# Kernel optimization log

Hardware: AMD Instinct MI355X
Metric: run time of the kernel (lower is better)

Reference implementation:

```python
import jax, jax.numpy as jnp
import numpy as np

KS = 5
SIGMA = 2.0
N_BINS = 50
MOMENTUM = 0.9
HALF_KS = (KS - 1) // 2


def _gaussian_kernel_window(ks=KS, sigma=SIGMA):
    # Replicates scipy.ndimage.gaussian_filter1d(delta, sigma, mode='reflect'),
    # then renormalizes, exactly as FDS._get_kernel_window does.
    half = (ks - 1) // 2
    base = np.zeros(ks, np.float32)
    base[half] = 1.0
    r = int(4.0 * sigma + 0.5)  # scipy default truncate=4.0
    j = np.arange(-r, r + 1)
    w = np.exp(-0.5 * (j / sigma) ** 2)
    w = w / w.sum()
    idx = np.arange(-r, ks + r)
    for _ in range(8):  # repeated 'reflect' (edge-excluding-center style: d c b a | a b c d | d c b a)
        idx = np.where(idx < 0, -idx - 1, idx)
        idx = np.where(idx >= ks, 2 * ks - 1 - idx, idx)
    xp = base[idx]
    out = np.array([float(np.dot(w, xp[i:i + 2 * r + 1])) for i in range(ks)], np.float32)
    return out / out.sum()


def setup_inputs() -> dict:
    key = jax.random.key(0)
    k1, k2, k3, k4 = jax.random.split(key, 4)
    N, D = 262144, 512
    features = jax.random.normal(k1, (N, D), dtype=jnp.float32)
    labels = jax.random.randint(k2, (N,), 0, N_BINS, dtype=jnp.int64)
    running_mean = jax.random.normal(k3, (N_BINS, D), dtype=jnp.float32)
    running_var = jax.random.uniform(k4, (N_BINS, D), dtype=jnp.float32) + 0.5
    num_samples_tracked = jnp.zeros((N_BINS,), dtype=jnp.float32)
    kernel_window = jnp.asarray(_gaussian_kernel_window(), dtype=jnp.float32)
    return {
        "features": features,
        "labels": labels,
        "running_mean": running_mean,
        "running_var": running_var,
        "num_samples_tracked": num_samples_tracked,
        "kernel_window": kernel_window,
    }


def _smooth(x, kernel_window):
    # reflect-pad (torch 'reflect': excludes edge) along bin axis, then cross-correlate (F.conv1d)
    top = x[HALF_KS:0:-1]              # [half_ks, D]
    bot = x[-2:-2 - HALF_KS:-1]        # [half_ks, D]
    xp = jnp.concatenate([top, x, bot], axis=0)  # [B + 2*half_ks, D]
    B = x.shape[0]
    windows = jnp.stack([xp[i:i + B] for i in range(KS)], axis=0)  # [ks, B, D]
    return jnp.einsum("k,kbd->bd", kernel_window, windows)


def reference(features, labels, running_mean, running_var, num_samples_tracked, kernel_window):
    # --- segmented per-bin mean/var (single pass, replaces the Python loop over labels) ---
    N = features.shape[0]
    labels = labels.astype(jnp.int32)
    counts = jax.ops.segment_sum(jnp.ones((N,), features.dtype), labels, num_segments=N_BINS)  # [B]
    sums = jax.ops.segment_sum(features, labels, num_segments=N_BINS)                          # [B, D]
    sumsq = jax.ops.segment_sum(features * features, labels, num_segments=N_BINS)              # [B, D]
    safe_n = jnp.maximum(counts, 1.0)
    mean = sums / safe_n[:, None]
    # unbiased var for n>1; biased (=0) for n==1, matching torch.var unbiased toggle
    var = (sumsq - safe_n[:, None] * mean * mean) / jnp.maximum(counts - 1.0, 1.0)[:, None]

    present = (counts > 0)[:, None]
    f = MOMENTUM
    new_mean = jnp.where(present, (1.0 - f) * mean + f * running_mean, running_mean)
    new_var = jnp.where(present, (1.0 - f) * var + f * running_var, running_var)
    new_num = num_samples_tracked + counts

    # --- update_smoothed_stats: conv1d smoothing over the bin axis ---
    smoothed_mean = _smooth(new_mean, kernel_window)
    smoothed_var = _smooth(new_var, kernel_window)
    return new_mean, new_var, new_num, smoothed_mean, smoothed_var
```

## Files before the change

kernel.cpp:

```cpp
#include <hip/hip_runtime.h>

#define NB 50
#define DD 512
#define KSZ 5
#define SORT_ROWS 4096
#define EPT 16
#define RPW 512
#define COLG 8
#define UNR 8

__global__ __launch_bounds__(256) void fds_sort(
    const int* __restrict__ labels,
    int*       __restrict__ packed,
    float*     __restrict__ g_cnt)
{
    __shared__ int s_hist[NB];
    __shared__ int s_cur[NB];
    const int tid  = threadIdx.x;
    const int base = blockIdx.x * SORT_ROWS;

    if (tid < NB) s_hist[tid] = 0;
    __syncthreads();

    int lab[EPT];
#pragma unroll
    for (int j = 0; j < EPT; ++j) {
        lab[j] = labels[base + j * 256 + tid];
        __hip_atomic_fetch_add(&s_hist[lab[j]], 1,
                               __ATOMIC_RELAXED, __HIP_MEMORY_SCOPE_WORKGROUP);
    }
    __syncthreads();

    if (tid == 0) {
        int run = 0;
        for (int b = 0; b < NB; ++b) { s_cur[b] = run; run += s_hist[b]; }
    }
    __syncthreads();

    if (tid < NB)
        __hip_atomic_fetch_add(&g_cnt[tid], (float)s_hist[tid],
                               __ATOMIC_RELAXED, __HIP_MEMORY_SCOPE_AGENT);

#pragma unroll
    for (int j = 0; j < EPT; ++j) {
        const int l   = lab[j];
        const int pos = __hip_atomic_fetch_add(&s_cur[l], 1,
                              __ATOMIC_RELAXED, __HIP_MEMORY_SCOPE_WORKGROUP);
        const int row = base + j * 256 + tid;
        packed[base + pos] = (row << 6) | l;
    }
}

__global__ __launch_bounds__(256) void fds_reduce(
    const float* __restrict__ features,
    const int*   __restrict__ packed,
    float* __restrict__ g_sum,
    float* __restrict__ g_sq)
{
    const int tid  = threadIdx.x;
    const int wave = tid >> 6;
    const int lane = tid & 63;
    const int gw   = blockIdx.x * 4 + wave;
    const int cg     = gw & (COLG - 1);
    const int rchunk = gw >> 3;
    const int col = cg * 64 + lane;
    const int r0  = rchunk * RPW;

    float sum = 0.f, sq = 0.f;
    int cur = packed[r0] & 63;

    int pk[UNR];
#pragma unroll
    for (int j = 0; j < UNR; ++j) pk[j] = packed[r0 + j];

    for (int it = 0; it < RPW; it += UNR) {
        float v[UNR];
#pragma unroll
        for (int j = 0; j < UNR; ++j)
            v[j] = features[(size_t)(pk[j] >> 6) * DD + col];

        int pk2[UNR];
        const int nb = (it + UNR < RPW) ? (r0 + it + UNR) : r0;
#pragma unroll
        for (int j = 0; j < UNR; ++j) pk2[j] = packed[nb + j];

#pragma unroll
        for (int j = 0; j < UNR; ++j) {
            const int l = pk[j] & 63;
            if (l != cur) {
                __hip_atomic_fetch_add(&g_sum[cur * DD + col], sum,
                                       __ATOMIC_RELAXED, __HIP_MEMORY_SCOPE_AGENT);
                __hip_atomic_fetch_add(&g_sq [cur * DD + col], sq,
                                       __ATOMIC_RELAXED, __HIP_MEMORY_SCOPE_AGENT);
                sum = 0.f; sq = 0.f; cur = l;
            }
            sum += v[j];
            sq = fmaf(v[j], v[j], sq);
        }
#pragma unroll
        for (int j = 0; j < UNR; ++j) pk[j] = pk2[j];
    }
    __hip_atomic_fetch_add(&g_sum[cur * DD + col], sum,
                           __ATOMIC_RELAXED, __HIP_MEMORY_SCOPE_AGENT);
    __hip_atomic_fetch_add(&g_sq [cur * DD + col], sq,
                           __ATOMIC_RELAXED, __HIP_MEMORY_SCOPE_AGENT);
}

__global__ __launch_bounds__(256) void fds_finalize(
    const float* __restrict__ g_sum, const float* __restrict__ g_sq,
    const float* __restrict__ g_cnt,
    const float* __restrict__ running_mean, const float* __restrict__ running_var,
    const float* __restrict__ num_tracked, const float* __restrict__ kwin,
    float* __restrict__ out)
{
    __shared__ float s_cnt[NB];
    __shared__ float s_w[KSZ];
    const int tid = threadIdx.x;
    if (tid < NB)  s_cnt[tid] = g_cnt[tid];
    if (tid < KSZ) s_w[tid]   = kwin[tid];
    __syncthreads();

    const int idx = blockIdx.x * 256 + tid;
    const int b = idx / DD;
    const int d = idx - b * DD;

    float sm = 0.f, sv = 0.f, my_nm = 0.f, my_nv = 0.f;
#pragma unroll
    for (int k = 0; k < KSZ; ++k) {
        const int i = b + k;
        const int bb = (i < 2) ? (2 - i) : ((i >= NB + 2) ? (2 * NB - i) : (i - 2));
        const float cnt    = s_cnt[bb];
        const float safe_n = fmaxf(cnt, 1.f);
        const float s   = g_sum[bb * DD + d];
        const float sqv = g_sq [bb * DD + d];
        const float mean = s / safe_n;
        const float var  = (sqv - safe_n * mean * mean) / fmaxf(cnt - 1.f, 1.f);
        const float rm = running_mean[bb * DD + d];
        const float rv = running_var [bb * DD + d];
        float nm, nv;
        if (cnt > 0.f) {
            nm = 0.1f * mean + 0.9f * rm;
            nv = 0.1f * var  + 0.9f * rv;
        } else {
            nm = rm; nv = rv;
        }
        sm += s_w[k] * nm;
        sv += s_w[k] * nv;
        if (k == 2) { my_nm = nm; my_nv = nv; }
    }
    out[idx]                    = my_nm;
    out[NB * DD + idx]          = my_nv;
    out[2 * NB * DD + NB + idx] = sm;
    out[3 * NB * DD + NB + idx] = sv;
    if (idx < NB)
        out[2 * NB * DD + idx] = num_tracked[idx] + s_cnt[idx];
}

extern "C" void kernel_launch(void* const* d_in, const int* in_sizes, int n_in,
                              void* d_out, int out_size, void* d_ws, size_t ws_size,
                              hipStream_t stream)
{
    const float* features     = (const float*)d_in[0];
    const int*   labels       = (const int*)  d_in[1];
    const float* running_mean = (const float*)d_in[2];
    const float* running_var  = (const float*)d_in[3];
    const float* num_tracked  = (const float*)d_in[4];
    const float* kwin         = (const float*)d_in[5];
    float* out = (float*)d_out;

    const int N = in_sizes[1];

    float* g_sum  = (float*)d_ws;
    float* g_sq   = g_sum + NB * DD;
    float* g_cnt  = g_sq  + NB * DD;
    int*   packed = (int*)(g_cnt + NB);

    hipMemsetAsync(d_ws, 0, (size_t)(2 * NB * DD + NB) * sizeof(float), stream);

    fds_sort<<<N / SORT_ROWS, 256, 0, stream>>>(labels, packed, g_cnt);

    fds_reduce<<<(N / RPW) * COLG / 4, 256, 0, stream>>>(features, packed, g_sum, g_sq);

    fds_finalize<<<NB * DD / 256, 256, 0, stream>>>(
        g_sum, g_sq, g_cnt, running_mean, running_var, num_tracked, kwin, out);
}
```

Baseline: 710.2 us.

## Vectorize reduce to float4 loads with nontemporal hints and shorter row chunks

Reworks the segmented reduction so each lane loads four contiguous columns as a float4, and one wave covers half a row (256 columns) instead of 64. Feature loads are marked nontemporal because the feature stream is read once. The rows per wave drop from 512 to 64 and the grid is resized to match. The aim is fewer, wider memory transactions and more parallelism for the 512 MB feature stream. In exchange, the shorter chunks produce more bin boundaries and so more global atomic flushes, four scalar atomics per accumulator each time.

New measurement: 709.4 us. Within noise of the previous version (-0.1%).

```diff
diff --git a/kernel.cpp b/kernel.cpp
--- a/kernel.cpp
+++ b/kernel.cpp
@@ -5,9 +5,10 @@
 #define KSZ 5
 #define SORT_ROWS 4096
 #define EPT 16
-#define RPW 512
-#define COLG 8
+#define RPW 64
 #define UNR 8
+
+typedef float f4 __attribute__((ext_vector_type(4)));
 
 __global__ __launch_bounds__(256) void fds_sort(
     const int* __restrict__ labels,
@@ -51,6 +52,21 @@
     }
 }
 
+__device__ __forceinline__ void flush4(
+    float* __restrict__ g_sum, float* __restrict__ g_sq,
+    int cur, int c0, f4 sum, f4 sq)
+{
+    float* ps = &g_sum[cur * DD + c0];
+    float* pq = &g_sq [cur * DD + c0];
+#pragma unroll
+    for (int c = 0; c < 4; ++c) {
+        __hip_atomic_fetch_add(ps + c, sum[c],
+                               __ATOMIC_RELAXED, __HIP_MEMORY_SCOPE_AGENT);
+        __hip_atomic_fetch_add(pq + c, sq[c],
+                               __ATOMIC_RELAXED, __HIP_MEMORY_SCOPE_AGENT);
+    }
+}
+
 __global__ __launch_bounds__(256) void fds_reduce(
     const float* __restrict__ features,
     const int*   __restrict__ packed,
@@ -61,12 +77,13 @@
     const int wave = tid >> 6;
     const int lane = tid & 63;
     const int gw   = blockIdx.x * 4 + wave;
-    const int cg     = gw & (COLG - 1);
-    const int rchunk = gw >> 3;
-    const int col = cg * 64 + lane;
+    const int cg2    = gw & 1;
+    const int rchunk = gw >> 1;
     const int r0  = rchunk * RPW;
+    const int c0  = cg2 * 256 + lane * 4;
+    const f4* __restrict__ f4p = (const f4*)features;
 
-    float sum = 0.f, sq = 0.f;
+    f4 sum = (f4)0.f, sq = (f4)0.f;
     int cur = packed[r0] & 63;
 
     int pk[UNR];
@@ -74,10 +91,11 @@
     for (int j = 0; j < UNR; ++j) pk[j] = packed[r0 + j];
 
     for (int it = 0; it < RPW; it += UNR) {
-        float v[UNR];
+        f4 v[UNR];
 #pragma unroll
         for (int j = 0; j < UNR; ++j)
-            v[j] = features[(size_t)(pk[j] >> 6) * DD + col];
+            v[j] = __builtin_nontemporal_load(
+                f4p + (size_t)(pk[j] >> 6) * (DD / 4) + cg2 * 64 + lane);
 
         int pk2[UNR];
         const int nb = (it + UNR < RPW) ? (r0 + it + UNR) : r0;
@@ -88,22 +106,16 @@
         for (int j = 0; j < UNR; ++j) {
             const int l = pk[j] & 63;
             if (l != cur) {
-                __hip_atomic_fetch_add(&g_sum[cur * DD + col], sum,
-                                       __ATOMIC_RELAXED, __HIP_MEMORY_SCOPE_AGENT);
-                __hip_atomic_fetch_add(&g_sq [cur * DD + col], sq,
-                                       __ATOMIC_RELAXED, __HIP_MEMORY_SCOPE_AGENT);
-                sum = 0.f; sq = 0.f; cur = l;
+                flush4(g_sum, g_sq, cur, c0, sum, sq);
+                sum = (f4)0.f; sq = (f4)0.f; cur = l;
             }
             sum += v[j];
-            sq = fmaf(v[j], v[j], sq);
+            sq  += v[j] * v[j];
         }
 #pragma unroll
         for (int j = 0; j < UNR; ++j) pk[j] = pk2[j];
     }
-    __hip_atomic_fetch_add(&g_sum[cur * DD + col], sum,
-                           __ATOMIC_RELAXED, __HIP_MEMORY_SCOPE_AGENT);
-    __hip_atomic_fetch_add(&g_sq [cur * DD + col], sq,
-                           __ATOMIC_RELAXED, __HIP_MEMORY_SCOPE_AGENT);
+    flush4(g_sum, g_sq, cur, c0, sum, sq);
 }
 
 __global__ __launch_bounds__(256) void fds_finalize(
@@ -179,7 +191,7 @@
 
     fds_sort<<<N / SORT_ROWS, 256, 0, stream>>>(labels, packed, g_cnt);
 
-    fds_reduce<<<(N / RPW) * COLG / 4, 256, 0, stream>>>(features, packed, g_sum, g_sq);
+    fds_reduce<<<(N / RPW) * 2 / 4, 256, 0, stream>>>(features, packed, g_sum, g_sq);
 
     fds_finalize<<<NB * DD / 256, 256, 0, stream>>>(
         g_sum, g_sq, g_cnt, running_mean, running_var, num_tracked, kwin, out);
```
